# Kernel optimization log

Measured on AMD Instinct MI355X. Metric: run time of the kernel, lower is better.

## Reference

```python
import jax, jax.numpy as jnp
import numpy as np

D_IN = 1024
D_OUT = 1024

def setup_inputs() -> dict:
    key = jax.random.key(0)
    kx, kq, kk, kv = jax.random.split(key, 4)
    x = jax.random.normal(kx, (4, 2048, D_IN), dtype=jnp.float32)
    # torch Linear weights are [d_out, d_in]; store as [d_in, d_out] for x @ W
    s = 1.0 / np.sqrt(D_IN)
    Wq = jax.random.uniform(kq, (D_IN, D_OUT), jnp.float32, -s, s)
    Wk = jax.random.uniform(kk, (D_IN, D_OUT), jnp.float32, -s, s)
    Wv = jax.random.uniform(kv, (D_IN, D_OUT), jnp.float32, -s, s)
    return {"x": x, "Wq": Wq, "Wk": Wk, "Wv": Wv}

def reference(x, Wq, Wk, Wv):
    # x: [b, n, d_in]
    n = x.shape[1]
    q = jnp.einsum('bnd,de->bne', x, Wq)
    k = jnp.einsum('bnd,de->bne', x, Wk)
    v = jnp.einsum('bnd,de->bne', x, Wv)
    scores = jnp.einsum('bqe,bke->bqk', q, k)  # [b, n, n]
    causal = jnp.tril(jnp.ones((n, n), dtype=bool))  # True = keep
    scores = jnp.where(causal, scores, -jnp.inf)
    attn = jax.nn.softmax(scores / jnp.sqrt(jnp.float32(k.shape[-1])), axis=-1)
    # dropout p=0.0 -> identity
    return jnp.einsum('bqk,bke->bqe', attn, v)
```

## Files before the change

### kernel.cpp

```cpp
#include <hip/hip_runtime.h>
#include <hip/hip_bf16.h>
#include <stdint.h>

#define D_ 1024
#define NSEQ 2048

typedef __attribute__((ext_vector_type(8))) short bf16x8;
typedef __attribute__((ext_vector_type(4))) float f32x4;

static __device__ __forceinline__ unsigned short f2bf(float x) {
    union { __hip_bfloat16 h; unsigned short u; } cv;
    cv.h = __float2bfloat16(x);
    return cv.u;
}

static __device__ __forceinline__ void gload_lds16(const void* g, void* l) {
    __builtin_amdgcn_global_load_lds(
        (const __attribute__((address_space(1))) unsigned int*)(uintptr_t)g,
        (__attribute__((address_space(3))) unsigned int*)(uintptr_t)l, 16, 0, 0);
}

__global__ __launch_bounds__(256) void cvt_x(const float* __restrict__ x,
                                             __hip_bfloat16* __restrict__ xb) {
    int i = blockIdx.x * 256 + threadIdx.x;
    float4 v = reinterpret_cast<const float4*>(x)[i];
    ushort4 o;
    o.x = f2bf(v.x); o.y = f2bf(v.y); o.z = f2bf(v.z); o.w = f2bf(v.w);
    reinterpret_cast<ushort4*>(xb)[i] = o;
}

__global__ __launch_bounds__(256) void wt_kernel(const float* __restrict__ Wq,
                                                 const float* __restrict__ Wk,
                                                 const float* __restrict__ Wv,
                                                 __hip_bfloat16* __restrict__ Wt) {
    const float* W = (blockIdx.z == 0) ? Wq : (blockIdx.z == 1) ? Wk : Wv;
    unsigned short* O = (unsigned short*)(Wt + (size_t)blockIdx.z * D_ * D_);
    __shared__ float tile[32][33];
    int r0 = blockIdx.y * 32, c0 = blockIdx.x * 32;
    int t = threadIdx.x;
    int r = t >> 3, c4 = (t & 7) * 4;
    float4 v = *reinterpret_cast<const float4*>(&W[(size_t)(r0 + r) * D_ + c0 + c4]);
    tile[r][c4 + 0] = v.x; tile[r][c4 + 1] = v.y;
    tile[r][c4 + 2] = v.z; tile[r][c4 + 3] = v.w;
    __syncthreads();
    int er = t >> 3, dc = (t & 7) * 4;
    ushort4 pk;
    pk.x = f2bf(tile[dc + 0][er]); pk.y = f2bf(tile[dc + 1][er]);
    pk.z = f2bf(tile[dc + 2][er]); pk.w = f2bf(tile[dc + 3][er]);
    *reinterpret_cast<ushort4*>(&O[(size_t)(c0 + er) * D_ + r0 + dc]) = pk;
}

template <int MODE>
__global__ __launch_bounds__(256) void gemm128(const __hip_bfloat16* __restrict__ A, int lda,
                                               const __hip_bfloat16* __restrict__ Bt, int ldb,
                                               void* __restrict__ o0, void* __restrict__ o1,
                                               void* __restrict__ o2,
                                               const float2* __restrict__ rl) {
    int bx, by, bz;
    if (MODE == 0) {
        bx = blockIdx.x; by = blockIdx.y; bz = 0;
    } else if (MODE == 2) {
        const int fid = blockIdx.x;
        bz = fid & 3;
        const int t = fid >> 2;
        bx = (int)((sqrtf(8.0f * t + 1.0f) - 1.0f) * 0.5f);
        while ((bx + 1) * (bx + 2) / 2 <= t) ++bx;
        while (bx * (bx + 1) / 2 > t) --bx;
        by = t - bx * (bx + 1) / 2;
    } else {
        const int fid = blockIdx.x;
        const int bxr = fid & 15;
        bx = (fid & 256) ? 15 - bxr : bxr;
        bz = (fid >> 4) & 3;
        by = fid >> 6;
    }

    const __hip_bfloat16* Ab = A;
    const __hip_bfloat16* Bb = Bt;
    int Kdim = 1024;
    if (MODE == 2) { Ab += (size_t)bz * NSEQ * D_;  Bb += (size_t)bz * NSEQ * D_; }
    if (MODE == 3) { Ab += (size_t)bz * NSEQ * 4096; Bb += (size_t)bz * D_ * NSEQ; Kdim = (bx + 1) * 128; }

    const int m0 = bx * 128, n0 = by * 128;

    __shared__ __hip_bfloat16 As[128 * 32];
    __shared__ __hip_bfloat16 Bs[128 * 32];

    const int tid = threadIdx.x;
    const int lane = tid & 63, wid = tid >> 6;
    const int wm = wid >> 1, wn = wid & 1;
    const int lr = lane & 15, lk = lane >> 4;

    const int srow = wid * 32 + (lane >> 2);
    const int scol = (lane & 3) * 8;
    const __hip_bfloat16* aptr = Ab + (size_t)(m0 + srow) * lda + scol;
    const __hip_bfloat16* bptr = Bb + (size_t)(n0 + srow) * ldb + scol;
    char* AsW = (char*)As + wid * 2048;
    char* BsW = (char*)Bs + wid * 2048;

    f32x4 acc[4][4] = {};

    for (int k0 = 0; k0 < Kdim; k0 += 32) {
        gload_lds16(aptr,                    AsW);
        gload_lds16(aptr + (size_t)16 * lda, AsW + 1024);
        gload_lds16(bptr,                    BsW);
        gload_lds16(bptr + (size_t)16 * ldb, BsW + 1024);
        aptr += 32; bptr += 32;
        __syncthreads();

        bf16x8 af[4], bfr[4];
#pragma unroll
        for (int m = 0; m < 4; ++m)
            af[m] = *reinterpret_cast<const bf16x8*>(&As[(wm * 64 + m * 16 + lr) * 32 + lk * 8]);
#pragma unroll
        for (int n = 0; n < 4; ++n)
            bfr[n] = *reinterpret_cast<const bf16x8*>(&Bs[(wn * 64 + n * 16 + lr) * 32 + lk * 8]);
#pragma unroll
        for (int m = 0; m < 4; ++m)
#pragma unroll
            for (int n = 0; n < 4; ++n)
                acc[m][n] = __builtin_amdgcn_mfma_f32_16x16x32_bf16(af[m], bfr[n], acc[m][n], 0, 0, 0);
        __syncthreads();
    }

    if (MODE == 0) {
#pragma unroll
        for (int m = 0; m < 4; ++m)
#pragma unroll
            for (int n = 0; n < 4; ++n) {
                const int rbase = m0 + wm * 64 + m * 16 + lk * 4;
                const int cbase = n0 + wn * 64 + n * 16 + lr;
                const int seg = cbase >> 10, e = cbase & 1023;
                if (seg < 2) {
                    unsigned short* C = (unsigned short*)(seg == 0 ? o0 : o1);
#pragma unroll
                    for (int j = 0; j < 4; ++j)
                        C[(size_t)(rbase + j) * D_ + e] = f2bf(acc[m][n][j]);
                } else {
                    unsigned short* Vt = (unsigned short*)o2;
                    const int b = rbase >> 11, nq = rbase & 2047;
                    ushort4 pk;
                    pk.x = f2bf(acc[m][n][0]); pk.y = f2bf(acc[m][n][1]);
                    pk.z = f2bf(acc[m][n][2]); pk.w = f2bf(acc[m][n][3]);
                    *reinterpret_cast<ushort4*>(&Vt[(((size_t)b << 10) + e) * NSEQ + nq]) = pk;
                }
            }
    } else if (MODE == 2) {
        float* S = (float*)o0 + (size_t)bz * NSEQ * NSEQ;
#pragma unroll
        for (int m = 0; m < 4; ++m)
#pragma unroll
            for (int n = 0; n < 4; ++n) {
                const int rbase = m0 + wm * 64 + m * 16 + lk * 4;
                const int cbase = n0 + wn * 64 + n * 16 + lr;
#pragma unroll
                for (int j = 0; j < 4; ++j) {
                    float s = acc[m][n][j] * 0.03125f;
                    if (cbase > rbase + j) s = -1e30f;
                    acc[m][n][j] = s;
                    S[(size_t)(rbase + j) * NSEQ + cbase] = s;
                }
            }
        float* Pm = (float*)o1;
        float* Pl = (float*)o2;
        const int pcol = by * 2 + wn;
#pragma unroll
        for (int m = 0; m < 4; ++m)
#pragma unroll
            for (int j = 0; j < 4; ++j) {
                float mx = fmaxf(fmaxf(acc[m][0][j], acc[m][1][j]),
                                 fmaxf(acc[m][2][j], acc[m][3][j]));
#pragma unroll
                for (int w = 1; w < 16; w <<= 1) mx = fmaxf(mx, __shfl_xor(mx, w, 64));
                float sm = __expf(acc[m][0][j] - mx) + __expf(acc[m][1][j] - mx) +
                           __expf(acc[m][2][j] - mx) + __expf(acc[m][3][j] - mx);
#pragma unroll
                for (int w = 1; w < 16; w <<= 1) sm += __shfl_xor(sm, w, 64);
                if (lr == 0) {
                    const int row = bz * NSEQ + m0 + wm * 64 + m * 16 + lk * 4 + j;
                    Pm[row * 32 + pcol] = mx;
                    Pl[row * 32 + pcol] = sm;
                }
            }
    } else {
        float* O = (float*)o0 + (size_t)bz * NSEQ * D_;
#pragma unroll
        for (int m = 0; m < 4; ++m)
#pragma unroll
            for (int n = 0; n < 4; ++n) {
                const int rbase = m0 + wm * 64 + m * 16 + lk * 4;
                const int cbase = n0 + wn * 64 + n * 16 + lr;
#pragma unroll
                for (int j = 0; j < 4; ++j)
                    O[(size_t)(rbase + j) * D_ + cbase] =
                        acc[m][n][j] * rl[bz * NSEQ + rbase + j].y;
            }
    }
}

__global__ __launch_bounds__(256) void softmax_finish(float* __restrict__ S,
                                                      const float* __restrict__ Pm,
                                                      const float* __restrict__ Pl,
                                                      float2* __restrict__ rl) {
    const int lane = threadIdx.x & 63;
    const int row = blockIdx.x * 4 + (threadIdx.x >> 6);
    const int q = row & 2047;
    const int nb = (q >> 7) + 1;
    const int nc = nb * 2;

    float mb = (lane < nc) ? Pm[row * 32 + lane] : -3e38f;
    float m = mb;
#pragma unroll
    for (int off = 32; off > 0; off >>= 1) m = fmaxf(m, __shfl_xor(m, off, 64));
    float lb = (lane < nc) ? Pl[row * 32 + lane] * __expf(mb - m) : 0.f;
#pragma unroll
    for (int off = 32; off > 0; off >>= 1) lb += __shfl_xor(lb, off, 64);
    if (lane == 0) rl[row] = make_float2(m, 1.0f / lb);

    float* srow = S + (size_t)row * NSEQ;
    unsigned short* prow = (unsigned short*)srow;
    const int L = nb << 7;
    for (int k = lane * 4; k < L; k += 256) {
        float4 v = *reinterpret_cast<const float4*>(srow + k);
        ushort4 pk;
        pk.x = f2bf(__expf(v.x - m)); pk.y = f2bf(__expf(v.y - m));
        pk.z = f2bf(__expf(v.z - m)); pk.w = f2bf(__expf(v.w - m));
        *reinterpret_cast<ushort4*>(prow + k) = pk;
    }
}

extern "C" void kernel_launch(void* const* d_in, const int* in_sizes, int n_in,
                              void* d_out, int out_size, void* d_ws, size_t ws_size,
                              hipStream_t stream) {
    const float* x  = (const float*)d_in[0];
    const float* Wq = (const float*)d_in[1];
    const float* Wk = (const float*)d_in[2];
    const float* Wv = (const float*)d_in[3];

    char* ws = (char*)d_ws;
    float*          S    = (float*)(ws);
    __hip_bfloat16* Xb   = (__hip_bfloat16*)(ws + 67108864);
    __hip_bfloat16* Q    = (__hip_bfloat16*)(ws + 83886080);
    __hip_bfloat16* K    = (__hip_bfloat16*)(ws + 100663296);
    __hip_bfloat16* Vt   = (__hip_bfloat16*)(ws + 117440512);
    __hip_bfloat16* Wt   = (__hip_bfloat16*)(ws + 134217728);
    float*  Pm = (float*)(ws + 67108864);
    float*  Pl = (float*)(ws + 68157440);
    float2* rl = (float2*)(ws + 69206016);

    cvt_x<<<8192, 256, 0, stream>>>(x, Xb);
    wt_kernel<<<dim3(32, 32, 3), 256, 0, stream>>>(Wq, Wk, Wv, Wt);

    gemm128<0><<<dim3(64, 24, 1), 256, 0, stream>>>(Xb, 1024, Wt, 1024, Q, K, Vt, nullptr);

    gemm128<2><<<dim3(544), 256, 0, stream>>>(Q, 1024, K, 1024, S, Pm, Pl, nullptr);
    softmax_finish<<<2048, 256, 0, stream>>>(S, Pm, Pl, rl);
    gemm128<3><<<dim3(512), 256, 0, stream>>>((const __hip_bfloat16*)S, 4096, Vt, 2048,
                                              d_out, nullptr, nullptr, rl);
}
```

Measured before the change: 175.4 us.

## Store scores as bf16, deepen GEMM K-tile to 64 with XOR-swizzled LDS

The score matrix is now written in bf16 rather than fp32, halving its write and read traffic in the softmax-finish pass and letting the PV GEMM read it with row stride 2048. The GEMM main loop processes K in 64-wide tiles with larger shared buffers and an XOR swizzle on LDS slots to avoid bank conflicts, which halves the number of barriers per K. Rounding scores to bf16 before exponentiation adds precision loss, and the doubled LDS footprint may reduce occupancy.

```diff
diff --git a/kernel.cpp b/kernel.cpp
--- a/kernel.cpp
+++ b/kernel.cpp
@@ -12,6 +12,11 @@
     union { __hip_bfloat16 h; unsigned short u; } cv;
     cv.h = __float2bfloat16(x);
     return cv.u;
+}
+static __device__ __forceinline__ float bf2f(unsigned short u) {
+    union { float f; unsigned int i; } cv;
+    cv.i = ((unsigned int)u) << 16;
+    return cv.f;
 }
 
 static __device__ __forceinline__ void gload_lds16(const void* g, void* l) {
@@ -78,48 +83,64 @@
     const __hip_bfloat16* Ab = A;
     const __hip_bfloat16* Bb = Bt;
     int Kdim = 1024;
-    if (MODE == 2) { Ab += (size_t)bz * NSEQ * D_;  Bb += (size_t)bz * NSEQ * D_; }
-    if (MODE == 3) { Ab += (size_t)bz * NSEQ * 4096; Bb += (size_t)bz * D_ * NSEQ; Kdim = (bx + 1) * 128; }
+    if (MODE == 2) { Ab += (size_t)bz * NSEQ * lda; Bb += (size_t)bz * NSEQ * ldb; }
+    if (MODE == 3) { Ab += (size_t)bz * NSEQ * lda; Bb += (size_t)bz * D_ * ldb; Kdim = (bx + 1) * 128; }
 
     const int m0 = bx * 128, n0 = by * 128;
 
-    __shared__ __hip_bfloat16 As[128 * 32];
-    __shared__ __hip_bfloat16 Bs[128 * 32];
+    __shared__ __hip_bfloat16 As[128 * 64];
+    __shared__ __hip_bfloat16 Bs[128 * 64];
 
     const int tid = threadIdx.x;
     const int lane = tid & 63, wid = tid >> 6;
     const int wm = wid >> 1, wn = wid & 1;
     const int lr = lane & 15, lk = lane >> 4;
 
-    const int srow = wid * 32 + (lane >> 2);
-    const int scol = (lane & 3) * 8;
-    const __hip_bfloat16* aptr = Ab + (size_t)(m0 + srow) * lda + scol;
-    const __hip_bfloat16* bptr = Bb + (size_t)(n0 + srow) * ldb + scol;
-    char* AsW = (char*)As + wid * 2048;
-    char* BsW = (char*)Bs + wid * 2048;
+    const __hip_bfloat16* asrc[4];
+    const __hip_bfloat16* bsrc[4];
+#pragma unroll
+    for (int r = 0; r < 4; ++r) {
+        const int chunk = r * 256 + tid;
+        const int row = chunk >> 3, slot = chunk & 7;
+        const int col = ((slot ^ (row & 7)) * 8);
+        asrc[r] = Ab + (size_t)(m0 + row) * lda + col;
+        bsrc[r] = Bb + (size_t)(n0 + row) * ldb + col;
+    }
+
+    const int sw = lr & 7;
+    const int slotA0 = (lk ^ sw) * 16, slotA1 = ((4 + lk) ^ sw) * 16;
 
     f32x4 acc[4][4] = {};
 
-    for (int k0 = 0; k0 < Kdim; k0 += 32) {
-        gload_lds16(aptr,                    AsW);
-        gload_lds16(aptr + (size_t)16 * lda, AsW + 1024);
-        gload_lds16(bptr,                    BsW);
-        gload_lds16(bptr + (size_t)16 * ldb, BsW + 1024);
-        aptr += 32; bptr += 32;
+    for (int k0 = 0; k0 < Kdim; k0 += 64) {
+#pragma unroll
+        for (int r = 0; r < 4; ++r) {
+            gload_lds16(asrc[r], (char*)As + r * 4096 + wid * 1024);
+            gload_lds16(bsrc[r], (char*)Bs + r * 4096 + wid * 1024);
+            asrc[r] += 64; bsrc[r] += 64;
+        }
         __syncthreads();
 
-        bf16x8 af[4], bfr[4];
-#pragma unroll
-        for (int m = 0; m < 4; ++m)
-            af[m] = *reinterpret_cast<const bf16x8*>(&As[(wm * 64 + m * 16 + lr) * 32 + lk * 8]);
-#pragma unroll
-        for (int n = 0; n < 4; ++n)
-            bfr[n] = *reinterpret_cast<const bf16x8*>(&Bs[(wn * 64 + n * 16 + lr) * 32 + lk * 8]);
+        bf16x8 af0[4], bf0[4], af1[4], bf1[4];
+#pragma unroll
+        for (int m = 0; m < 4; ++m) {
+            const int ra = (wm * 64 + m * 16 + lr) * 128;
+            const int rb = (wn * 64 + m * 16 + lr) * 128;
+            af0[m] = *reinterpret_cast<const bf16x8*>((const char*)As + ra + slotA0);
+            af1[m] = *reinterpret_cast<const bf16x8*>((const char*)As + ra + slotA1);
+            bf0[m] = *reinterpret_cast<const bf16x8*>((const char*)Bs + rb + slotA0);
+            bf1[m] = *reinterpret_cast<const bf16x8*>((const char*)Bs + rb + slotA1);
+        }
 #pragma unroll
         for (int m = 0; m < 4; ++m)
 #pragma unroll
             for (int n = 0; n < 4; ++n)
-                acc[m][n] = __builtin_amdgcn_mfma_f32_16x16x32_bf16(af[m], bfr[n], acc[m][n], 0, 0, 0);
+                acc[m][n] = __builtin_amdgcn_mfma_f32_16x16x32_bf16(af0[m], bf0[n], acc[m][n], 0, 0, 0);
+#pragma unroll
+        for (int m = 0; m < 4; ++m)
+#pragma unroll
+            for (int n = 0; n < 4; ++n)
+                acc[m][n] = __builtin_amdgcn_mfma_f32_16x16x32_bf16(af1[m], bf1[n], acc[m][n], 0, 0, 0);
         __syncthreads();
     }
 
@@ -146,7 +167,7 @@
                 }
             }
     } else if (MODE == 2) {
-        float* S = (float*)o0 + (size_t)bz * NSEQ * NSEQ;
+        unsigned short* S = (unsigned short*)o0 + (size_t)bz * NSEQ * NSEQ;
 #pragma unroll
         for (int m = 0; m < 4; ++m)
 #pragma unroll
@@ -158,7 +179,7 @@
                     float s = acc[m][n][j] * 0.03125f;
                     if (cbase > rbase + j) s = -1e30f;
                     acc[m][n][j] = s;
-                    S[(size_t)(rbase + j) * NSEQ + cbase] = s;
+                    S[(size_t)(rbase + j) * NSEQ + cbase] = f2bf(s);
                 }
             }
         float* Pm = (float*)o1;
@@ -198,7 +219,7 @@
     }
 }
 
-__global__ __launch_bounds__(256) void softmax_finish(float* __restrict__ S,
+__global__ __launch_bounds__(256) void softmax_finish(unsigned short* __restrict__ S,
                                                       const float* __restrict__ Pm,
                                                       const float* __restrict__ Pl,
                                                       float2* __restrict__ rl) {
@@ -217,15 +238,18 @@
     for (int off = 32; off > 0; off >>= 1) lb += __shfl_xor(lb, off, 64);
     if (lane == 0) rl[row] = make_float2(m, 1.0f / lb);
 
-    float* srow = S + (size_t)row * NSEQ;
-    unsigned short* prow = (unsigned short*)srow;
+    unsigned short* srow = S + (size_t)row * NSEQ;
     const int L = nb << 7;
-    for (int k = lane * 4; k < L; k += 256) {
-        float4 v = *reinterpret_cast<const float4*>(srow + k);
-        ushort4 pk;
-        pk.x = f2bf(__expf(v.x - m)); pk.y = f2bf(__expf(v.y - m));
-        pk.z = f2bf(__expf(v.z - m)); pk.w = f2bf(__expf(v.w - m));
-        *reinterpret_cast<ushort4*>(prow + k) = pk;
+    for (int k = lane * 8; k < L; k += 512) {
+        ushort4 a = *reinterpret_cast<const ushort4*>(srow + k);
+        ushort4 b = *reinterpret_cast<const ushort4*>(srow + k + 4);
+        ushort4 pa, pb;
+        pa.x = f2bf(__expf(bf2f(a.x) - m)); pa.y = f2bf(__expf(bf2f(a.y) - m));
+        pa.z = f2bf(__expf(bf2f(a.z) - m)); pa.w = f2bf(__expf(bf2f(a.w) - m));
+        pb.x = f2bf(__expf(bf2f(b.x) - m)); pb.y = f2bf(__expf(bf2f(b.y) - m));
+        pb.z = f2bf(__expf(bf2f(b.z) - m)); pb.w = f2bf(__expf(bf2f(b.w) - m));
+        *reinterpret_cast<ushort4*>(srow + k)     = pa;
+        *reinterpret_cast<ushort4*>(srow + k + 4) = pb;
     }
 }
 
@@ -238,7 +262,7 @@
     const float* Wv = (const float*)d_in[3];
 
     char* ws = (char*)d_ws;
-    float*          S    = (float*)(ws);
+    unsigned short* S    = (unsigned short*)(ws);
     __hip_bfloat16* Xb   = (__hip_bfloat16*)(ws + 67108864);
     __hip_bfloat16* Q    = (__hip_bfloat16*)(ws + 83886080);
     __hip_bfloat16* K    = (__hip_bfloat16*)(ws + 100663296);
@@ -255,6 +279,6 @@
 
     gemm128<2><<<dim3(544), 256, 0, stream>>>(Q, 1024, K, 1024, S, Pm, Pl, nullptr);
     softmax_finish<<<2048, 256, 0, stream>>>(S, Pm, Pl, rl);
-    gemm128<3><<<dim3(512), 256, 0, stream>>>((const __hip_bfloat16*)S, 4096, Vt, 2048,
+    gemm128<3><<<dim3(512), 256, 0, stream>>>((const __hip_bfloat16*)S, 2048, Vt, 2048,
                                               d_out, nullptr, nullptr, rl);
 }
```

Result: faster. 169.7 us (-3.2%).
